# Kernel optimization log

Measured on AMD Instinct MI355X. Metric: run time of the kernel, lower is better.

## Reference

```python
import jax, jax.numpy as jnp
import numpy as np
import math

B, L, DM = 2, 256, 256
H, NK, T = 8, 4, 4  # heads, num_kernels, time_dim
DH = DM // H


def _gauss_mean_over_d(t, mu, sigma, w):
    """t: [B,P,T]; mu/sigma/w: [H,D,T,K] -> mean over D of sum_{t,k} w*exp(...): [B,H,P].
    Scans over D to avoid materializing [B,H,D,P,T,K]."""
    D = mu.shape[1]

    def step(acc, p):
        mu_d, sg_d, w_d = p  # each [H,T,K]
        diff = t[:, None, :, :, None] - mu_d[None, :, None, :, :]  # [B,H,P,T,K]
        g = (w_d[None, :, None] * jnp.exp(-diff ** 2 / (2.0 * sg_d[None, :, None] ** 2))).sum((-1, -2))
        return acc + g, None

    init = jnp.zeros((t.shape[0], mu.shape[0], t.shape[1]), t.dtype)
    params = (jnp.moveaxis(mu, 1, 0), jnp.moveaxis(sigma, 1, 0), jnp.moveaxis(w, 1, 0))
    acc, _ = jax.lax.scan(jax.checkpoint(step), init, params)
    return acc / D


def setup_inputs() -> dict:
    key = jax.random.key(0)
    ks = jax.random.split(key, 16)
    s = 1.0 / math.sqrt(DM)
    return {
        "x": jax.random.normal(ks[0], (B, L, DM), jnp.float32),
        "t": jax.random.uniform(ks[1], (B, L, T), jnp.float32),
        "WQ": jax.random.normal(ks[2], (DM, DM), jnp.float32) * s,
        "WK": jax.random.normal(ks[3], (DM, DM), jnp.float32) * s,
        "WV": jax.random.normal(ks[4], (DM, DM), jnp.float32) * s,
        "WO": jax.random.normal(ks[5], (DM, DM), jnp.float32) * s,
        "bO": jnp.zeros((DM,), jnp.float32),
        "mu_abs": jax.random.normal(ks[6], (H, DH, T, NK), jnp.float32),
        "sigma_abs": jnp.abs(jax.random.normal(ks[7], (H, DH, T, NK), jnp.float32)) + 1e-5,
        "w_abs": jax.random.normal(ks[8], (H, DH, T, NK), jnp.float32),
        "mu_rel": jax.random.normal(ks[9], (H, DH, T, NK), jnp.float32),
        "sigma_rel": jnp.abs(jax.random.normal(ks[10], (H, DH, T, NK), jnp.float32)) + 1e-5,
        "w_rel": jax.random.normal(ks[11], (H, DH, T, NK), jnp.float32),
        "alpha": jnp.ones((H,), jnp.float32),
        "beta": jnp.ones((H,), jnp.float32),
        "gamma": jnp.zeros((H,), jnp.float32),
    }


def reference(x, t, WQ, WK, WV, WO, bO, mu_abs, sigma_abs, w_abs,
              mu_rel, sigma_rel, w_rel, alpha, beta, gamma):
    b, l, dm = x.shape
    h = alpha.shape[0]
    dh = dm // h

    def heads(y):  # [B,L,DM] -> [B,H,L,DH]
        return y.reshape(b, l, h, dh).transpose(0, 2, 1, 3)

    Q = heads(x @ WQ.T)
    K = heads(x @ WK.T)
    V = heads(x @ WV.T)
    Xh = heads(x)

    Pij = jnp.einsum('bhid,bhjd->bhij', Xh, Xh)

    g_abs = _gauss_mean_over_d(t, mu_abs, sigma_abs, w_abs)  # [B,H,L]
    t_rel = jnp.abs(t[:, :, None, :] - t[:, None, :, :]).reshape(b, l * l, t.shape[-1])
    g_rel = _gauss_mean_over_d(t_rel, mu_rel, sigma_rel, w_rel).reshape(b, h, l, l)

    gi = g_abs[:, :, :, None]  # [B,H,L,1]
    a = alpha[None, :, None, None]
    bb = beta[None, :, None, None]
    c = gamma[None, :, None, None]
    # original: g_abs_j = g_abs_i broadcast over j, so (g_i + g_j) == 2*gi broadcast
    A = a * Pij * (gi + gi) + bb * Pij * g_rel + c

    scores = jnp.einsum('bhid,bhjd->bhij', Q, K) / math.sqrt(dh)
    attn = jax.nn.softmax(scores * A, axis=-1)  # dropout = identity (eval)
    out = jnp.einsum('bhij,bhjd->bhid', attn, V)
    out = out.transpose(0, 2, 1, 3).reshape(b, l, dm)
    return out @ WO.T + bO
```

## Files before the change

### kernel.cpp

```cpp
#include <hip/hip_runtime.h>
#include <math.h>

constexpr int Bc = 2, Lc = 256, DMc = 256, Hc = 8, DHc = 32;
constexpr float LOG2E = 1.4426950408889634f;
constexpr float RSQRT_DH = 0.17677669529663687f;
#define EXP2 __builtin_amdgcn_exp2f

constexpr int   NTAB = 512;
constexpr float SIG0 = 0.02f;

__device__ __forceinline__ float mixsum(const float4* __restrict__ prm, float x) {
    float acc = 0.f;
    #pragma unroll 8
    for (int q = 0; q < 128; ++q) {
        float4 p = prm[q];
        float d0 = x - p.x;
        acc = fmaf(p.z, EXP2(d0 * d0 * p.y), acc);
    }
    return acc;
}

__device__ __forceinline__ void role_tab(int bx,
    const float* __restrict__ mu, const float* __restrict__ sg, const float* __restrict__ w,
    float4* __restrict__ TAB, float4* __restrict__ NLIST, int* __restrict__ NCNT,
    float* smem)
{
    float4* prm = (float4*)smem;
    float*  fs  = smem + 512;
    int*    lcnt = (int*)(smem + 772);
    int hm = bx >> 2, chunk = bx & 3;
    int h = hm >> 2, tau = hm & 3;
    int tid = threadIdx.x;

    if (tid == 0) *lcnt = 0;
    __syncthreads();
    if (tid < 128) {
        int d = tid >> 2, k = tid & 3;
        int off = h * 512 + d * 16 + tau * 4 + k;
        float s  = sg[off];
        float mv = mu[off], wv = w[off];
        float n = -(0.5f * LOG2E) / (s * s);
        bool narrow = (s < SIG0);
        prm[tid] = make_float4(mv, n, narrow ? 0.0f : wv, 0.0f);
        if (chunk == 0 && narrow) {
            int slot = atomicAdd(lcnt, 1);
            NLIST[hm * 128 + slot] = make_float4(mv, n, wv, 0.0f);
        }
    }
    __syncthreads();
    if (chunk == 0 && tid == 0) NCNT[hm] = *lcnt;

    fs[tid] = mixsum(prm, (float)(chunk * 256 + tid) * (1.0f / 1024.0f));
    if (tid == 0)
        fs[256] = mixsum(prm, (float)(chunk * 256 + 256) * (1.0f / 1024.0f));
    __syncthreads();

    if (tid < 128) {
        float f0 = fs[tid * 2], fm = fs[tid * 2 + 1], f1 = fs[tid * 2 + 2];
        float c2 = 2.0f * (f0 + f1 - 2.0f * fm);
        float c1 = f1 - f0 - c2;
        TAB[hm * NTAB + chunk * 128 + tid] = make_float4(f0, c1, c2, 0.0f);
    }
}

__device__ __forceinline__ void role_gabs(int idx, const float* __restrict__ t,
                                          const float* __restrict__ mu, const float* __restrict__ sg,
                                          const float* __restrict__ w, float* __restrict__ gabs,
                                          float* smem) {
    int h = idx & 7, b = (idx >> 3) & 1, q = idx >> 4;
    int tid = threadIdx.x;
    {
        float2 s2 = *(const float2*)(sg + h * 512 + tid * 2);
        float2 o;
        o.x = -(0.5f * LOG2E) / (s2.x * s2.x);
        o.y = -(0.5f * LOG2E) / (s2.y * s2.y);
        *(float2*)(smem + tid * 2) = o;
    }
    __syncthreads();
    int lane = tid & 63, tg = tid >> 6;
    int i = q * 64 + lane;
    float tv = t[(b * Lc + i) * 4 + tg];
    const float* muB = mu + h * 512 + tg * 4;
    const float* wB  = w  + h * 512 + tg * 4;
    const float* nsB = smem + tg * 4;
    float acc = 0.f;
    #pragma unroll 4
    for (int d = 0; d < 32; ++d) {
        float4 m4 = *(const float4*)(muB + d * 16);
        float4 w4 = *(const float4*)(wB  + d * 16);
        float4 n4 = *(const float4*)(nsB + d * 16);
        float d0 = tv - m4.x; acc = fmaf(w4.x, EXP2(d0 * d0 * n4.x), acc);
        float d1 = tv - m4.y; acc = fmaf(w4.y, EXP2(d1 * d1 * n4.y), acc);
        float d2 = tv - m4.z; acc = fmaf(w4.z, EXP2(d2 * d2 * n4.z), acc);
        float d3 = tv - m4.w; acc = fmaf(w4.w, EXP2(d3 * d3 * n4.w), acc);
    }
    float* red = smem + 512;
    red[tg * 64 + lane] = acc;
    __syncthreads();
    if (tid < 64)
        gabs[(b * Hc + h) * Lc + q * 64 + lane] =
            (red[lane] + red[64 + lane] + red[128 + lane] + red[192 + lane]) * (1.0f / 32.0f);
}

template<int R>
__device__ __forceinline__ void stage_tile2(const float* __restrict__ src, int ld,
                                            int row0, int k0, float* __restrict__ dst, int tid) {
    int row = tid >> 3;
    int cb = (tid & 7) * 2;
    float2 v = *(const float2*)(src + (size_t)(row0 + row) * ld + k0 + cb);
    dst[(cb + 0) * (R + 1) + row] = v.x;
    dst[(cb + 1) * (R + 1) + row] = v.y;
}

__device__ __forceinline__ void gemm32(const float* __restrict__ A, const float* __restrict__ W,
                                       float* __restrict__ C, const float* __restrict__ bias,
                                       float sc, int m0, int n0, float* smem) {
    float* As = smem;
    float* Ws = smem + 16 * 33;
    int tid = threadIdx.x;
    int tx = tid & 15, ty = tid >> 4;
    float acc[2][2] = {};
    for (int k0 = 0; k0 < 256; k0 += 16) {
        stage_tile2<32>(A, 256, m0, k0, As, tid);
        stage_tile2<32>(W, 256, n0, k0, Ws, tid);
        __syncthreads();
        #pragma unroll
        for (int k = 0; k < 16; ++k) {
            float a0 = As[k * 33 + ty * 2], a1 = As[k * 33 + ty * 2 + 1];
            float w0 = Ws[k * 33 + tx * 2], w1 = Ws[k * 33 + tx * 2 + 1];
            acc[0][0] = fmaf(a0, w0, acc[0][0]);
            acc[0][1] = fmaf(a0, w1, acc[0][1]);
            acc[1][0] = fmaf(a1, w0, acc[1][0]);
            acc[1][1] = fmaf(a1, w1, acc[1][1]);
        }
        __syncthreads();
    }
    #pragma unroll
    for (int u = 0; u < 2; ++u) {
        int m = m0 + ty * 2 + u;
        #pragma unroll
        for (int v = 0; v < 2; ++v) {
            float o = acc[u][v] * sc;
            if (bias) o += bias[n0 + tx * 2 + v];
            C[(size_t)m * DMc + n0 + tx * 2 + v] = o;
        }
    }
}

__global__ void __launch_bounds__(256) k_pre(
    const float* __restrict__ x, const float* __restrict__ t,
    const float* __restrict__ WQ, const float* __restrict__ WK, const float* __restrict__ WV,
    const float* __restrict__ mu_a, const float* __restrict__ sg_a, const float* __restrict__ w_a,
    const float* __restrict__ mu_r, const float* __restrict__ sg_r, const float* __restrict__ w_r,
    float* __restrict__ Qb, float* __restrict__ Kb, float* __restrict__ Vb,
    float* __restrict__ GA,
    float4* __restrict__ TAB, float4* __restrict__ NLIST, int* __restrict__ NCNT)
{
    __shared__ __align__(16) float smem[1056];
    int bx = blockIdx.x;
    if (bx < 128) {
        role_tab(bx, mu_r, sg_r, w_r, TAB, NLIST, NCNT, smem);
    } else if (bx < 192) {
        role_gabs(bx - 128, t, mu_a, sg_a, w_a, GA, smem);
    } else {
        int idx = bx - 192;
        int z = idx >> 7;
        int r = idx & 127;
        int m0 = (r >> 3) * 32, n0 = (r & 7) * 32;
        const float* W = (z == 0) ? WQ : (z == 1) ? WK : WV;
        float* C = (z == 0) ? Qb : (z == 1) ? Kb : Vb;
        gemm32(x, W, C, nullptr, (z == 0) ? RSQRT_DH : 1.0f, m0, n0, smem);
    }
}

__global__ void __launch_bounds__(512) k_sp(
    const float* __restrict__ Q, const float* __restrict__ K, const float* __restrict__ x,
    const float* __restrict__ t, const float* __restrict__ gabs,
    const float4* __restrict__ TAB, const float4* __restrict__ NLIST,
    const int* __restrict__ NCNT,
    const float* __restrict__ alpha, const float* __restrict__ beta, const float* __restrict__ gamma,
    float* __restrict__ G)
{
    constexpr int PITCH = 68;
    int it = blockIdx.x, jt = blockIdx.y, bh = blockIdx.z;
    int b = bh >> 3, h = bh & 7;
    int i0 = it * 64, j0 = jt * 64;
    int tid = threadIdx.x;
    __shared__ __align__(16) float sm[4 * 32 * PITCH];
    float* sQ  = sm;
    float* sK  = sm + 32 * PITCH;
    float* sXi = sm + 64 * PITCH;
    float* sXj = sm + 96 * PITCH;

    {
        int r = tid >> 3;
        int c4 = (tid & 7) * 4;
        float4 qv = *(const float4*)(Q + ((size_t)(b * Lc + i0 + r) * DMc + h * DHc + c4));
        float4 kv = *(const float4*)(K + ((size_t)(b * Lc + j0 + r) * DMc + h * DHc + c4));
        float4 xi = *(const float4*)(x + ((size_t)(b * Lc + i0 + r) * DMc + h * DHc + c4));
        float4 xj = *(const float4*)(x + ((size_t)(b * Lc + j0 + r) * DMc + h * DHc + c4));
        const float* q_ = (const float*)&qv; const float* k_ = (const float*)&kv;
        const float* a_ = (const float*)&xi; const float* c_ = (const float*)&xj;
        #pragma unroll
        for (int u = 0; u < 4; ++u) {
            sQ [(c4 + u) * PITCH + r] = q_[u];
            sK [(c4 + u) * PITCH + r] = k_[u];
            sXi[(c4 + u) * PITCH + r] = a_[u];
            sXj[(c4 + u) * PITCH + r] = c_[u];
        }
    }
    __syncthreads();

    int tx = tid & 15, ty = tid >> 4;
    int i2 = ty * 2, j4 = tx * 4;
    float accS[2][4] = {}, accP[2][4] = {};
    #pragma unroll 4
    for (int k = 0; k < 32; ++k) {
        float2 qa = *(const float2*)(sQ  + k * PITCH + i2);
        float4 kb = *(const float4*)(sK  + k * PITCH + j4);
        float2 xa = *(const float2*)(sXi + k * PITCH + i2);
        float4 xb = *(const float4*)(sXj + k * PITCH + j4);
        const float* qa_ = (const float*)&qa; const float* kb_ = (const float*)&kb;
        const float* xa_ = (const float*)&xa; const float* xb_ = (const float*)&xb;
        #pragma unroll
        for (int u = 0; u < 2; ++u)
            #pragma unroll
            for (int v = 0; v < 4; ++v) {
                accS[u][v] = fmaf(qa_[u], kb_[v], accS[u][v]);
                accP[u][v] = fmaf(xa_[u], xb_[v], accP[u][v]);
            }
    }

    __syncthreads();
    float4* tab = (float4*)sm;
    {
        const float4* src = TAB + (size_t)h * 4 * NTAB;
        #pragma unroll
        for (int u = 0; u < 4; ++u)
            tab[tid + u * 512] = src[tid + u * 512];
    }
    __syncthreads();

    float4 tiv[2], tjv[4];
    #pragma unroll
    for (int u = 0; u < 2; ++u)
        tiv[u] = *(const float4*)(t + (size_t)(b * Lc + i0 + i2 + u) * 4);
    #pragma unroll
    for (int v = 0; v < 4; ++v)
        tjv[v] = *(const float4*)(t + (size_t)(b * Lc + j0 + j4 + v) * 4);

    float g8[2][4] = {};
    #pragma unroll
    for (int tg = 0; tg < 4; ++tg) {
        float xv[2][4];
        #pragma unroll
        for (int u = 0; u < 2; ++u) {
            float tiu = ((const float*)&tiv[u])[tg];
            #pragma unroll
            for (int v = 0; v < 4; ++v) {
                float xx = fabsf(tiu - ((const float*)&tjv[v])[tg]);
                xv[u][v] = xx;
                float xs = xx * (float)NTAB;
                int iu = min((int)xs, NTAB - 1);
                float uu = xs - (float)iu;
                float4 c = tab[tg * NTAB + iu];
                g8[u][v] += fmaf(uu, fmaf(uu, c.z, c.y), c.x);
            }
        }
        int cn = NCNT[h * 4 + tg];
        for (int nn = 0; nn < cn; ++nn) {
            float4 q = NLIST[(h * 4 + tg) * 128 + nn];
            #pragma unroll
            for (int u = 0; u < 2; ++u)
                #pragma unroll
                for (int v = 0; v < 4; ++v) {
                    float d0 = xv[u][v] - q.x;
                    g8[u][v] = fmaf(q.z, EXP2(d0 * d0 * q.y), g8[u][v]);
                }
        }
    }

    float la = alpha[h], lb = beta[h], lg = gamma[h];
    constexpr float SC = 1.0f / 32.0f;
    float* gb = G + (size_t)bh * (Lc * Lc);
    #pragma unroll
    for (int u = 0; u < 2; ++u) {
        int i = i0 + i2 + u;
        float gi2 = 2.0f * la * gabs[bh * Lc + i];
        float* addr = gb + (size_t)i * Lc + j0 + j4;
        float4 o;
        o.x = accS[u][0] * fmaf(accP[u][0], fmaf(lb, g8[u][0] * SC, gi2), lg);
        o.y = accS[u][1] * fmaf(accP[u][1], fmaf(lb, g8[u][1] * SC, gi2), lg);
        o.z = accS[u][2] * fmaf(accP[u][2], fmaf(lb, g8[u][2] * SC, gi2), lg);
        o.w = accS[u][3] * fmaf(accP[u][3], fmaf(lb, g8[u][3] * SC, gi2), lg);
        *(float4*)addr = o;
    }
}

__global__ void __launch_bounds__(512) k_pvsm(const float* __restrict__ P,
                                              const float* __restrict__ V,
                                              float* __restrict__ AO) {
    int it = blockIdx.x, bh = blockIdx.y;
    int b = bh >> 3, h = bh & 7;
    int i0 = it * 16;
    int tid = threadIdx.x;
    __shared__ float sP[16 * 260];
    __shared__ float sV[256 * 34];
    int i = tid >> 5, l = tid & 31;

    const float* row = P + (size_t)bh * (Lc * Lc) + (size_t)(i0 + i) * Lc + l * 8;
    float4 p0 = *(const float4*)(row);
    float4 p1 = *(const float4*)(row + 4);
    float m = fmaxf(fmaxf(fmaxf(p0.x, p0.y), fmaxf(p0.z, p0.w)),
                    fmaxf(fmaxf(p1.x, p1.y), fmaxf(p1.z, p1.w)));
    #pragma unroll
    for (int s = 1; s < 32; s <<= 1) m = fmaxf(m, __shfl_xor(m, s, 32));
    float4 e0, e1;
    e0.x = EXP2((p0.x - m) * LOG2E); e0.y = EXP2((p0.y - m) * LOG2E);
    e0.z = EXP2((p0.z - m) * LOG2E); e0.w = EXP2((p0.w - m) * LOG2E);
    e1.x = EXP2((p1.x - m) * LOG2E); e1.y = EXP2((p1.y - m) * LOG2E);
    e1.z = EXP2((p1.z - m) * LOG2E); e1.w = EXP2((p1.w - m) * LOG2E);
    float sum = ((e0.x + e0.y) + (e0.z + e0.w)) + ((e1.x + e1.y) + (e1.z + e1.w));
    #pragma unroll
    for (int s = 1; s < 32; s <<= 1) sum += __shfl_xor(sum, s, 32);
    float rs = 1.0f / sum;
    *(float4*)(sP + i * 260 + l * 8)     = e0;
    *(float4*)(sP + i * 260 + l * 8 + 4) = e1;

    {
        int jr = tid >> 3, c4 = (tid & 7) * 4;
        #pragma unroll
        for (int u = 0; u < 4; ++u) {
            int j = jr + u * 64;
            *(float4*)(sV + j * 34 + c4) =
                *(const float4*)(V + ((size_t)(b * Lc + j) * DMc + h * DHc + c4));
        }
    }
    __syncthreads();

    int d = l;
    float o0 = 0.f;
    #pragma unroll 4
    for (int j4 = 0; j4 < 256; j4 += 4) {
        float4 p4 = *(const float4*)(sP + i * 260 + j4);
        float v0 = sV[(j4 + 0) * 34 + d];
        float v1 = sV[(j4 + 1) * 34 + d];
        float v2 = sV[(j4 + 2) * 34 + d];
        float v3 = sV[(j4 + 3) * 34 + d];
        o0 = fmaf(p4.x, v0, o0); o0 = fmaf(p4.y, v1, o0);
        o0 = fmaf(p4.z, v2, o0); o0 = fmaf(p4.w, v3, o0);
    }
    AO[((size_t)(b * Lc + i0 + i) * DMc + h * DHc + d)] = o0 * rs;
}

__global__ void __launch_bounds__(256) k_out(const float* __restrict__ A,
                                             const float* __restrict__ W,
                                             const float* __restrict__ bias,
                                             float* __restrict__ C) {
    __shared__ float smem[2 * 16 * 33];
    gemm32(A, W, C, bias, 1.0f, blockIdx.x * 32, blockIdx.y * 32, smem);
}

extern "C" void kernel_launch(void* const* d_in, const int* in_sizes, int n_in,
                              void* d_out, int out_size, void* d_ws, size_t ws_size,
                              hipStream_t stream) {
    (void)in_sizes; (void)n_in; (void)out_size; (void)ws_size;
    const float* x      = (const float*)d_in[0];
    const float* t      = (const float*)d_in[1];
    const float* WQ     = (const float*)d_in[2];
    const float* WK     = (const float*)d_in[3];
    const float* WV     = (const float*)d_in[4];
    const float* WO     = (const float*)d_in[5];
    const float* bO     = (const float*)d_in[6];
    const float* mu_abs = (const float*)d_in[7];
    const float* sg_abs = (const float*)d_in[8];
    const float* w_abs  = (const float*)d_in[9];
    const float* mu_rel = (const float*)d_in[10];
    const float* sg_rel = (const float*)d_in[11];
    const float* w_rel  = (const float*)d_in[12];
    const float* alpha  = (const float*)d_in[13];
    const float* beta   = (const float*)d_in[14];
    const float* gamma  = (const float*)d_in[15];
    float* out = (float*)d_out;
    float* ws = (float*)d_ws;

    float* Qb = ws;
    float* Kb = ws + 131072;
    float* Vb = ws + 262144;
    float* AO = ws + 393216;
    float* GA = ws + 524288;
    float* GR = ws + 528384;
    float4* TAB   = (float4*)(ws + 1576960);
    float4* NLIST = (float4*)(ws + 1642496);
    int*    NCNT  = (int*)   (ws + 1658880);

    k_pre<<<dim3(576), dim3(256), 0, stream>>>(x, t, WQ, WK, WV,
                                               mu_abs, sg_abs, w_abs,
                                               mu_rel, sg_rel, w_rel,
                                               Qb, Kb, Vb, GA, TAB, NLIST, NCNT);
    k_sp<<<dim3(4, 4, 16), dim3(512), 0, stream>>>(Qb, Kb, x, t, GA,
                                                   TAB, NLIST, NCNT,
                                                   alpha, beta, gamma, GR);
    k_pvsm<<<dim3(16, 16), dim3(512), 0, stream>>>(GR, Vb, AO);
    k_out<<<dim3(16, 8), dim3(256), 0, stream>>>(AO, WO, bO, out);
}
```

Before: 124.7 us.

## Use 64x64 register-blocked GEMM tiles and split interpolation table into planar arrays

The QKV and output projections move from 32x32 tiles with 2x2 per-thread outputs to 64x64 tiles with 4x4 outputs, loaded with float4 from global and shared memory. This halves the k_pre block count and quarters the k_out grid. The relative-Gaussian quadratic table is also stored as three separate coefficient planes instead of float4 records, which changes how k_sp reads it from shared memory. More reuse per thread comes at the cost of far fewer blocks on a large GPU: only 32 for the output GEMM and 96 for QKV, which lowers parallelism.

```diff
diff --git a/kernel.cpp b/kernel.cpp
--- a/kernel.cpp
+++ b/kernel.cpp
@@ -22,7 +22,7 @@
 
 __device__ __forceinline__ void role_tab(int bx,
     const float* __restrict__ mu, const float* __restrict__ sg, const float* __restrict__ w,
-    float4* __restrict__ TAB, float4* __restrict__ NLIST, int* __restrict__ NCNT,
+    float* __restrict__ TABf, float4* __restrict__ NLIST, int* __restrict__ NCNT,
     float* smem)
 {
     float4* prm = (float4*)smem;
@@ -59,7 +59,10 @@
         float f0 = fs[tid * 2], fm = fs[tid * 2 + 1], f1 = fs[tid * 2 + 2];
         float c2 = 2.0f * (f0 + f1 - 2.0f * fm);
         float c1 = f1 - f0 - c2;
-        TAB[hm * NTAB + chunk * 128 + tid] = make_float4(f0, c1, c2, 0.0f);
+        int o = hm * NTAB + chunk * 128 + tid;
+        TABf[o]         = f0;
+        TABf[16384 + o] = c1;
+        TABf[32768 + o] = c2;
     }
 }
 
@@ -102,47 +105,55 @@
             (red[lane] + red[64 + lane] + red[128 + lane] + red[192 + lane]) * (1.0f / 32.0f);
 }
 
-template<int R>
-__device__ __forceinline__ void stage_tile2(const float* __restrict__ src, int ld,
-                                            int row0, int k0, float* __restrict__ dst, int tid) {
-    int row = tid >> 3;
-    int cb = (tid & 7) * 2;
-    float2 v = *(const float2*)(src + (size_t)(row0 + row) * ld + k0 + cb);
-    dst[(cb + 0) * (R + 1) + row] = v.x;
-    dst[(cb + 1) * (R + 1) + row] = v.y;
-}
-
-__device__ __forceinline__ void gemm32(const float* __restrict__ A, const float* __restrict__ W,
+__device__ __forceinline__ void gemm64(const float* __restrict__ A,
+                                       const float* __restrict__ W,
                                        float* __restrict__ C, const float* __restrict__ bias,
                                        float sc, int m0, int n0, float* smem) {
+    constexpr int GP = 68;
     float* As = smem;
-    float* Ws = smem + 16 * 33;
+    float* Ws = smem + 32 * GP;
     int tid = threadIdx.x;
     int tx = tid & 15, ty = tid >> 4;
-    float acc[2][2] = {};
-    for (int k0 = 0; k0 < 256; k0 += 16) {
-        stage_tile2<32>(A, 256, m0, k0, As, tid);
-        stage_tile2<32>(W, 256, n0, k0, Ws, tid);
+    int r = tid >> 3;
+    int c4 = (tid & 7) * 4;
+    float acc[4][4] = {};
+    for (int k0 = 0; k0 < 256; k0 += 32) {
+        #pragma unroll
+        for (int half = 0; half < 2; ++half) {
+            int row = r + half * 32;
+            float4 av = *(const float4*)(A + (size_t)(m0 + row) * DMc + k0 + c4);
+            float4 wv = *(const float4*)(W + (size_t)(n0 + row) * DMc + k0 + c4);
+            const float* a_ = (const float*)&av;
+            const float* w_ = (const float*)&wv;
+            #pragma unroll
+            for (int u = 0; u < 4; ++u) {
+                As[(c4 + u) * GP + row] = a_[u];
+                Ws[(c4 + u) * GP + row] = w_[u];
+            }
+        }
         __syncthreads();
-        #pragma unroll
-        for (int k = 0; k < 16; ++k) {
-            float a0 = As[k * 33 + ty * 2], a1 = As[k * 33 + ty * 2 + 1];
-            float w0 = Ws[k * 33 + tx * 2], w1 = Ws[k * 33 + tx * 2 + 1];
-            acc[0][0] = fmaf(a0, w0, acc[0][0]);
-            acc[0][1] = fmaf(a0, w1, acc[0][1]);
-            acc[1][0] = fmaf(a1, w0, acc[1][0]);
-            acc[1][1] = fmaf(a1, w1, acc[1][1]);
+        #pragma unroll 8
+        for (int k = 0; k < 32; ++k) {
+            float4 a4 = *(const float4*)(As + k * GP + ty * 4);
+            float4 w4 = *(const float4*)(Ws + k * GP + tx * 4);
+            const float* a_ = (const float*)&a4;
+            const float* w_ = (const float*)&w4;
+            #pragma unroll
+            for (int u = 0; u < 4; ++u)
+                #pragma unroll
+                for (int v = 0; v < 4; ++v)
+                    acc[u][v] = fmaf(a_[u], w_[v], acc[u][v]);
         }
         __syncthreads();
     }
     #pragma unroll
-    for (int u = 0; u < 2; ++u) {
-        int m = m0 + ty * 2 + u;
-        #pragma unroll
-        for (int v = 0; v < 2; ++v) {
+    for (int u = 0; u < 4; ++u) {
+        int m = m0 + ty * 4 + u;
+        #pragma unroll
+        for (int v = 0; v < 4; ++v) {
             float o = acc[u][v] * sc;
-            if (bias) o += bias[n0 + tx * 2 + v];
-            C[(size_t)m * DMc + n0 + tx * 2 + v] = o;
+            if (bias) o += bias[n0 + tx * 4 + v];
+            C[(size_t)m * DMc + n0 + tx * 4 + v] = o;
         }
     }
 }
@@ -154,29 +165,31 @@
     const float* __restrict__ mu_r, const float* __restrict__ sg_r, const float* __restrict__ w_r,
     float* __restrict__ Qb, float* __restrict__ Kb, float* __restrict__ Vb,
     float* __restrict__ GA,
-    float4* __restrict__ TAB, float4* __restrict__ NLIST, int* __restrict__ NCNT)
+    float* __restrict__ TABf, float4* __restrict__ NLIST, int* __restrict__ NCNT)
 {
-    __shared__ __align__(16) float smem[1056];
+    __shared__ __align__(16) float smem[2 * 32 * 68];
     int bx = blockIdx.x;
     if (bx < 128) {
-        role_tab(bx, mu_r, sg_r, w_r, TAB, NLIST, NCNT, smem);
+        role_tab(bx, mu_r, sg_r, w_r, TABf, NLIST, NCNT, smem);
     } else if (bx < 192) {
         role_gabs(bx - 128, t, mu_a, sg_a, w_a, GA, smem);
     } else {
         int idx = bx - 192;
-        int z = idx >> 7;
-        int r = idx & 127;
-        int m0 = (r >> 3) * 32, n0 = (r & 7) * 32;
+        int mt = idx / 12, nt = idx - mt * 12;
+        int m0 = mt * 64;
+        int n0g = nt * 64;
+        int z = n0g >> 8;
+        int n0 = n0g & 255;
         const float* W = (z == 0) ? WQ : (z == 1) ? WK : WV;
         float* C = (z == 0) ? Qb : (z == 1) ? Kb : Vb;
-        gemm32(x, W, C, nullptr, (z == 0) ? RSQRT_DH : 1.0f, m0, n0, smem);
+        gemm64(x, W, C, nullptr, (z == 0) ? RSQRT_DH : 1.0f, m0, n0, smem);
     }
 }
 
 __global__ void __launch_bounds__(512) k_sp(
     const float* __restrict__ Q, const float* __restrict__ K, const float* __restrict__ x,
     const float* __restrict__ t, const float* __restrict__ gabs,
-    const float4* __restrict__ TAB, const float4* __restrict__ NLIST,
+    const float* __restrict__ TABf, const float4* __restrict__ NLIST,
     const int* __restrict__ NCNT,
     const float* __restrict__ alpha, const float* __restrict__ beta, const float* __restrict__ gamma,
     float* __restrict__ G)
@@ -232,12 +245,16 @@
     }
 
     __syncthreads();
-    float4* tab = (float4*)sm;
+    float* sc0 = sm;
+    float* sc1 = sm + 2048;
+    float* sc2 = sm + 4096;
     {
-        const float4* src = TAB + (size_t)h * 4 * NTAB;
-        #pragma unroll
-        for (int u = 0; u < 4; ++u)
-            tab[tid + u * 512] = src[tid + u * 512];
+        const float4* p0 = (const float4*)(TABf + (size_t)h * 2048);
+        const float4* p1 = (const float4*)(TABf + 16384 + (size_t)h * 2048);
+        const float4* p2 = (const float4*)(TABf + 32768 + (size_t)h * 2048);
+        ((float4*)sc0)[tid] = p0[tid];
+        ((float4*)sc1)[tid] = p1[tid];
+        ((float4*)sc2)[tid] = p2[tid];
     }
     __syncthreads();
 
@@ -263,8 +280,11 @@
                 float xs = xx * (float)NTAB;
                 int iu = min((int)xs, NTAB - 1);
                 float uu = xs - (float)iu;
-                float4 c = tab[tg * NTAB + iu];
-                g8[u][v] += fmaf(uu, fmaf(uu, c.z, c.y), c.x);
+                int base = tg * NTAB + iu;
+                float v0 = sc0[base];
+                float v1 = sc1[base];
+                float v2 = sc2[base];
+                g8[u][v] += fmaf(uu, fmaf(uu, v2, v1), v0);
             }
         }
         int cn = NCNT[h * 4 + tg];
@@ -357,8 +377,9 @@
                                              const float* __restrict__ W,
                                              const float* __restrict__ bias,
                                              float* __restrict__ C) {
-    __shared__ float smem[2 * 16 * 33];
-    gemm32(A, W, C, bias, 1.0f, blockIdx.x * 32, blockIdx.y * 32, smem);
+    __shared__ __align__(16) float smem[2 * 32 * 68];
+    int mt = blockIdx.x >> 2, nt = blockIdx.x & 3;
+    gemm64(A, W, C, bias, 1.0f, mt * 64, nt * 64, smem);
 }
 
 extern "C" void kernel_launch(void* const* d_in, const int* in_sizes, int n_in,
@@ -390,17 +411,17 @@
     float* AO = ws + 393216;
     float* GA = ws + 524288;
     float* GR = ws + 528384;
-    float4* TAB   = (float4*)(ws + 1576960);
+    float* TABf   = ws + 1576960;
     float4* NLIST = (float4*)(ws + 1642496);
     int*    NCNT  = (int*)   (ws + 1658880);
 
-    k_pre<<<dim3(576), dim3(256), 0, stream>>>(x, t, WQ, WK, WV,
+    k_pre<<<dim3(288), dim3(256), 0, stream>>>(x, t, WQ, WK, WV,
                                                mu_abs, sg_abs, w_abs,
                                                mu_rel, sg_rel, w_rel,
-                                               Qb, Kb, Vb, GA, TAB, NLIST, NCNT);
+                                               Qb, Kb, Vb, GA, TABf, NLIST, NCNT);
     k_sp<<<dim3(4, 4, 16), dim3(512), 0, stream>>>(Qb, Kb, x, t, GA,
-                                                   TAB, NLIST, NCNT,
+                                                   TABf, NLIST, NCNT,
                                                    alpha, beta, gamma, GR);
     k_pvsm<<<dim3(16, 16), dim3(512), 0, stream>>>(GR, Vb, AO);
-    k_out<<<dim3(16, 8), dim3(256), 0, stream>>>(AO, WO, bO, out);
-}
+    k_out<<<dim3(32), dim3(256), 0, stream>>>(AO, WO, bO, out);
+}
```

After: 136.4 us. +9.4%, slower.

## Fuse score computation, softmax and PV into one attention kernel

Applied to the files above, without the earlier changes.

Merges the score/bias kernel and the softmax+PV kernel into a single kernel where each block handles 16 query rows against all 256 keys, computing scores, the Gaussian relative bias, softmax and the V product in shared memory. This removes the round trip of the full B*H*L*L score matrix through global memory and one kernel launch. In exchange each block recomputes the X_j projection tile over all keys and uses a large shared allocation (~89KB), which lowers occupancy. An extra barrier is also added in the gabs role before reusing shared memory.

```diff
diff --git a/kernel.cpp b/kernel.cpp
--- a/kernel.cpp
+++ b/kernel.cpp
@@ -95,6 +95,7 @@
         float d3 = tv - m4.w; acc = fmaf(w4.w, EXP2(d3 * d3 * n4.w), acc);
     }
     float* red = smem + 512;
+    __syncthreads();
     red[tg * 64 + lane] = acc;
     __syncthreads();
     if (tid < 64)
@@ -173,53 +174,54 @@
     }
 }
 
-__global__ void __launch_bounds__(512) k_sp(
+__global__ void __launch_bounds__(512) k_att(
     const float* __restrict__ Q, const float* __restrict__ K, const float* __restrict__ x,
     const float* __restrict__ t, const float* __restrict__ gabs,
     const float4* __restrict__ TAB, const float4* __restrict__ NLIST,
     const int* __restrict__ NCNT,
     const float* __restrict__ alpha, const float* __restrict__ beta, const float* __restrict__ gamma,
-    float* __restrict__ G)
+    const float* __restrict__ V, float* __restrict__ AO)
 {
-    constexpr int PITCH = 68;
-    int it = blockIdx.x, jt = blockIdx.y, bh = blockIdx.z;
+    __shared__ __align__(16) float sm[22224];
+    float* sK  = sm;
+    float* sXj = sm + 8704;
+    float* sQ  = sm + 17408;
+    float* sP  = sm + 18048;
+    float* sRS = sm + 22208;
+
+    int it = blockIdx.x, bh = blockIdx.y;
     int b = bh >> 3, h = bh & 7;
-    int i0 = it * 64, j0 = jt * 64;
+    int i0 = it * 16;
     int tid = threadIdx.x;
-    __shared__ __align__(16) float sm[4 * 32 * PITCH];
-    float* sQ  = sm;
-    float* sK  = sm + 32 * PITCH;
-    float* sXi = sm + 64 * PITCH;
-    float* sXj = sm + 96 * PITCH;
 
     {
-        int r = tid >> 3;
-        int c4 = (tid & 7) * 4;
-        float4 qv = *(const float4*)(Q + ((size_t)(b * Lc + i0 + r) * DMc + h * DHc + c4));
-        float4 kv = *(const float4*)(K + ((size_t)(b * Lc + j0 + r) * DMc + h * DHc + c4));
-        float4 xi = *(const float4*)(x + ((size_t)(b * Lc + i0 + r) * DMc + h * DHc + c4));
-        float4 xj = *(const float4*)(x + ((size_t)(b * Lc + j0 + r) * DMc + h * DHc + c4));
-        const float* q_ = (const float*)&qv; const float* k_ = (const float*)&kv;
-        const float* a_ = (const float*)&xi; const float* c_ = (const float*)&xj;
+        int r = tid >> 3, c4 = (tid & 7) * 4;
         #pragma unroll
         for (int u = 0; u < 4; ++u) {
-            sQ [(c4 + u) * PITCH + r] = q_[u];
-            sK [(c4 + u) * PITCH + r] = k_[u];
-            sXi[(c4 + u) * PITCH + r] = a_[u];
-            sXj[(c4 + u) * PITCH + r] = c_[u];
-        }
-    }
-    __syncthreads();
-
-    int tx = tid & 15, ty = tid >> 4;
+            int j = r + u * 64;
+            float4 kv = *(const float4*)(K + ((size_t)(b * Lc + j) * DMc + h * DHc + c4));
+            float4 xj = *(const float4*)(x + ((size_t)(b * Lc + j) * DMc + h * DHc + c4));
+            const float* k_ = (const float*)&kv; const float* x_ = (const float*)&xj;
+            #pragma unroll
+            for (int q = 0; q < 4; ++q) {
+                sK [(c4 + q) * 264 + j] = k_[q];
+                sXj[(c4 + q) * 264 + j] = x_[q];
+            }
+        }
+        int i = tid >> 5, k = tid & 31;
+        sQ[k * 20 + i] = Q[((size_t)(b * Lc + i0 + i) * DMc + h * DHc + k)];
+    }
+    __syncthreads();
+
+    int tx = tid & 63, ty = tid >> 6;
     int i2 = ty * 2, j4 = tx * 4;
     float accS[2][4] = {}, accP[2][4] = {};
     #pragma unroll 4
     for (int k = 0; k < 32; ++k) {
-        float2 qa = *(const float2*)(sQ  + k * PITCH + i2);
-        float4 kb = *(const float4*)(sK  + k * PITCH + j4);
-        float2 xa = *(const float2*)(sXi + k * PITCH + i2);
-        float4 xb = *(const float4*)(sXj + k * PITCH + j4);
+        float2 qa = *(const float2*)(sQ  + k * 20  + i2);
+        float2 xa = *(const float2*)(sXj + k * 264 + i0 + i2);
+        float4 kb = *(const float4*)(sK  + k * 264 + j4);
+        float4 xb = *(const float4*)(sXj + k * 264 + j4);
         const float* qa_ = (const float*)&qa; const float* kb_ = (const float*)&kb;
         const float* xa_ = (const float*)&xa; const float* xb_ = (const float*)&xb;
         #pragma unroll
@@ -230,10 +232,17 @@
                 accP[u][v] = fmaf(xa_[u], xb_[v], accP[u][v]);
             }
     }
-
-    __syncthreads();
-    float4* tab = (float4*)sm;
+    __syncthreads();
+
     {
+        int jr = tid >> 3, c4 = (tid & 7) * 4;
+        #pragma unroll
+        for (int u = 0; u < 4; ++u) {
+            int j = jr + u * 64;
+            *(float4*)(sK + j * 34 + c4) =
+                *(const float4*)(V + ((size_t)(b * Lc + j) * DMc + h * DHc + c4));
+        }
+        float4* tab = (float4*)sXj;
         const float4* src = TAB + (size_t)h * 4 * NTAB;
         #pragma unroll
         for (int u = 0; u < 4; ++u)
@@ -241,13 +250,14 @@
     }
     __syncthreads();
 
+    float4* tab = (float4*)sXj;
     float4 tiv[2], tjv[4];
     #pragma unroll
     for (int u = 0; u < 2; ++u)
         tiv[u] = *(const float4*)(t + (size_t)(b * Lc + i0 + i2 + u) * 4);
     #pragma unroll
     for (int v = 0; v < 4; ++v)
-        tjv[v] = *(const float4*)(t + (size_t)(b * Lc + j0 + j4 + v) * 4);
+        tjv[v] = *(const float4*)(t + (size_t)(b * Lc + j4 + v) * 4);
 
     float g8[2][4] = {};
     #pragma unroll
@@ -282,82 +292,48 @@
 
     float la = alpha[h], lb = beta[h], lg = gamma[h];
     constexpr float SC = 1.0f / 32.0f;
-    float* gb = G + (size_t)bh * (Lc * Lc);
     #pragma unroll
     for (int u = 0; u < 2; ++u) {
-        int i = i0 + i2 + u;
-        float gi2 = 2.0f * la * gabs[bh * Lc + i];
-        float* addr = gb + (size_t)i * Lc + j0 + j4;
-        float4 o;
-        o.x = accS[u][0] * fmaf(accP[u][0], fmaf(lb, g8[u][0] * SC, gi2), lg);
-        o.y = accS[u][1] * fmaf(accP[u][1], fmaf(lb, g8[u][1] * SC, gi2), lg);
-        o.z = accS[u][2] * fmaf(accP[u][2], fmaf(lb, g8[u][2] * SC, gi2), lg);
-        o.w = accS[u][3] * fmaf(accP[u][3], fmaf(lb, g8[u][3] * SC, gi2), lg);
-        *(float4*)addr = o;
-    }
-}
-
-__global__ void __launch_bounds__(512) k_pvsm(const float* __restrict__ P,
-                                              const float* __restrict__ V,
-                                              float* __restrict__ AO) {
-    int it = blockIdx.x, bh = blockIdx.y;
-    int b = bh >> 3, h = bh & 7;
-    int i0 = it * 16;
-    int tid = threadIdx.x;
-    __shared__ float sP[16 * 260];
-    __shared__ float sV[256 * 34];
-    int i = tid >> 5, l = tid & 31;
-
-    const float* row = P + (size_t)bh * (Lc * Lc) + (size_t)(i0 + i) * Lc + l * 8;
-    float4 p0 = *(const float4*)(row);
-    float4 p1 = *(const float4*)(row + 4);
-    float m = fmaxf(fmaxf(fmaxf(p0.x, p0.y), fmaxf(p0.z, p0.w)),
-                    fmaxf(fmaxf(p1.x, p1.y), fmaxf(p1.z, p1.w)));
-    #pragma unroll
-    for (int s = 1; s < 32; s <<= 1) m = fmaxf(m, __shfl_xor(m, s, 32));
-    float4 e0, e1;
-    e0.x = EXP2((p0.x - m) * LOG2E); e0.y = EXP2((p0.y - m) * LOG2E);
-    e0.z = EXP2((p0.z - m) * LOG2E); e0.w = EXP2((p0.w - m) * LOG2E);
-    e1.x = EXP2((p1.x - m) * LOG2E); e1.y = EXP2((p1.y - m) * LOG2E);
-    e1.z = EXP2((p1.z - m) * LOG2E); e1.w = EXP2((p1.w - m) * LOG2E);
-    float sum = ((e0.x + e0.y) + (e0.z + e0.w)) + ((e1.x + e1.y) + (e1.z + e1.w));
-    #pragma unroll
-    for (int s = 1; s < 32; s <<= 1) sum += __shfl_xor(sum, s, 32);
-    float rs = 1.0f / sum;
-    *(float4*)(sP + i * 260 + l * 8)     = e0;
-    *(float4*)(sP + i * 260 + l * 8 + 4) = e1;
+        float gi2 = 2.0f * la * gabs[bh * Lc + i0 + i2 + u];
+        float l0 = accS[u][0] * fmaf(accP[u][0], fmaf(lb, g8[u][0] * SC, gi2), lg);
+        float l1 = accS[u][1] * fmaf(accP[u][1], fmaf(lb, g8[u][1] * SC, gi2), lg);
+        float l2 = accS[u][2] * fmaf(accP[u][2], fmaf(lb, g8[u][2] * SC, gi2), lg);
+        float l3 = accS[u][3] * fmaf(accP[u][3], fmaf(lb, g8[u][3] * SC, gi2), lg);
+        float m = fmaxf(fmaxf(l0, l1), fmaxf(l2, l3));
+        #pragma unroll
+        for (int s = 1; s < 64; s <<= 1) m = fmaxf(m, __shfl_xor(m, s, 64));
+        float4 e;
+        e.x = EXP2((l0 - m) * LOG2E); e.y = EXP2((l1 - m) * LOG2E);
+        e.z = EXP2((l2 - m) * LOG2E); e.w = EXP2((l3 - m) * LOG2E);
+        float su = (e.x + e.y) + (e.z + e.w);
+        #pragma unroll
+        for (int s = 1; s < 64; s <<= 1) su += __shfl_xor(su, s, 64);
+        *(float4*)(sP + (i2 + u) * 260 + j4) = e;
+        if (tx == 0) sRS[i2 + u] = 1.0f / su;
+    }
+    __syncthreads();
 
     {
-        int jr = tid >> 3, c4 = (tid & 7) * 4;
-        #pragma unroll
-        for (int u = 0; u < 4; ++u) {
-            int j = jr + u * 64;
-            *(float4*)(sV + j * 34 + c4) =
-                *(const float4*)(V + ((size_t)(b * Lc + j) * DMc + h * DHc + c4));
-        }
-    }
-    __syncthreads();
-
-    int d = l;
-    float o0 = 0.f;
-    #pragma unroll 4
-    for (int j4 = 0; j4 < 256; j4 += 4) {
-        float4 p4 = *(const float4*)(sP + i * 260 + j4);
-        float v0 = sV[(j4 + 0) * 34 + d];
-        float v1 = sV[(j4 + 1) * 34 + d];
-        float v2 = sV[(j4 + 2) * 34 + d];
-        float v3 = sV[(j4 + 3) * 34 + d];
-        o0 = fmaf(p4.x, v0, o0); o0 = fmaf(p4.y, v1, o0);
-        o0 = fmaf(p4.z, v2, o0); o0 = fmaf(p4.w, v3, o0);
-    }
-    AO[((size_t)(b * Lc + i0 + i) * DMc + h * DHc + d)] = o0 * rs;
+        int i = tid >> 5, d = tid & 31;
+        float rs = sRS[i];
+        float o0 = 0.f;
+        #pragma unroll 4
+        for (int jj = 0; jj < 256; jj += 4) {
+            float4 p4 = *(const float4*)(sP + i * 260 + jj);
+            o0 = fmaf(p4.x, sK[(jj + 0) * 34 + d], o0);
+            o0 = fmaf(p4.y, sK[(jj + 1) * 34 + d], o0);
+            o0 = fmaf(p4.z, sK[(jj + 2) * 34 + d], o0);
+            o0 = fmaf(p4.w, sK[(jj + 3) * 34 + d], o0);
+        }
+        AO[((size_t)(b * Lc + i0 + i) * DMc + h * DHc + d)] = o0 * rs;
+    }
 }
 
 __global__ void __launch_bounds__(256) k_out(const float* __restrict__ A,
                                              const float* __restrict__ W,
                                              const float* __restrict__ bias,
                                              float* __restrict__ C) {
-    __shared__ float smem[2 * 16 * 33];
+    __shared__ __align__(16) float smem[1056];
     gemm32(A, W, C, bias, 1.0f, blockIdx.x * 32, blockIdx.y * 32, smem);
 }
 
@@ -389,7 +365,6 @@
     float* Vb = ws + 262144;
     float* AO = ws + 393216;
     float* GA = ws + 524288;
-    float* GR = ws + 528384;
     float4* TAB   = (float4*)(ws + 1576960);
     float4* NLIST = (float4*)(ws + 1642496);
     int*    NCNT  = (int*)   (ws + 1658880);
@@ -398,9 +373,8 @@
                                                mu_abs, sg_abs, w_abs,
                                                mu_rel, sg_rel, w_rel,
                                                Qb, Kb, Vb, GA, TAB, NLIST, NCNT);
-    k_sp<<<dim3(4, 4, 16), dim3(512), 0, stream>>>(Qb, Kb, x, t, GA,
-                                                   TAB, NLIST, NCNT,
-                                                   alpha, beta, gamma, GR);
-    k_pvsm<<<dim3(16, 16), dim3(512), 0, stream>>>(GR, Vb, AO);
+    k_att<<<dim3(16, 16), dim3(512), 0, stream>>>(Qb, Kb, x, t, GA,
+                                                  TAB, NLIST, NCNT,
+                                                  alpha, beta, gamma, Vb, AO);
     k_out<<<dim3(16, 8), dim3(256), 0, stream>>>(AO, WO, bO, out);
 }
```

Result: no change. 124.6 us, median of 2 (-0.1%).
